# Performance work log

Hardware: AMD Instinct MI355X
Metric: run time of the kernel (lower is better)

Reference implementation:

```python
import jax, jax.numpy as jnp
import numpy as np

B, N, D_IN, D_OUT, E = 16, 16384, 128, 128, 65536
LN_EPS = 1e-5


def setup_inputs() -> dict:
    key = jax.random.key(0)
    k1, k2, k3, k4 = jax.random.split(key, 4)
    x = jax.random.normal(k1, (B, N, D_IN), dtype=jnp.float32)
    edge_index = jax.random.randint(k2, (2, E), 0, N, dtype=jnp.int64)
    W_self = jax.random.normal(k3, (D_OUT, D_IN), dtype=jnp.float32) / np.sqrt(D_IN)
    W_neigh = jax.random.normal(k4, (D_OUT, D_IN), dtype=jnp.float32) / np.sqrt(D_IN)
    return {
        "x": x,
        "edge_index": edge_index,
        "batch_size": B,
        "W_self": W_self,
        "W_neigh": W_neigh,
        "bias": jnp.zeros((D_OUT,), jnp.float32),
        "gamma": jnp.ones((D_OUT,), jnp.float32),
        "beta": jnp.zeros((D_OUT,), jnp.float32),
    }


def reference(x, edge_index, batch_size, W_self, W_neigh, bias, gamma, beta):
    b, n, d = x.shape
    src, dst = edge_index[0], edge_index[1]
    # expand edge index for disjoint batched graphs: add per-graph node offsets
    offsets = (jnp.arange(batch_size, dtype=src.dtype) * n)[:, None]  # [B,1]
    src_e = (src[None, :] + offsets).reshape(-1)  # [B*E]
    dst_e = (dst[None, :] + offsets).reshape(-1)
    x_flat = x.reshape(batch_size * n, d)
    # scatter-sum neighbor features and degrees, then mean
    agg = jax.ops.segment_sum(x_flat[src_e], dst_e, num_segments=batch_size * n)
    deg = jax.ops.segment_sum(jnp.ones_like(dst_e, dtype=x_flat.dtype), dst_e,
                              num_segments=batch_size * n)
    neigh = agg / jnp.maximum(deg, 1.0)[:, None]
    out = x_flat @ W_self.T + neigh @ W_neigh.T + bias  # [B*N, D_OUT]
    # LayerNorm over last dim
    mu = jnp.mean(out, axis=-1, keepdims=True)
    var = jnp.mean(jnp.square(out - mu), axis=-1, keepdims=True)
    out = (out - mu) * jax.lax.rsqrt(var + LN_EPS) * gamma + beta
    out = jax.nn.relu(out)
    return out.reshape(batch_size, n, -1)
```

## Files before the change

### kernel.cpp

```cpp
#include <hip/hip_runtime.h>
#include <hip/hip_bf16.h>
#include <stdint.h>

#define B_ 16
#define N_ 16384
#define D_ 128
#define E_ 65536

typedef __attribute__((ext_vector_type(8))) __bf16 bf16x8;
typedef __attribute__((ext_vector_type(4))) float f32x4;
typedef __attribute__((ext_vector_type(4))) _Float16 half4;

__device__ __forceinline__ uint16_t f2bf(float f) {
    union { float f; uint32_t u; } v;
    v.f = f;
    uint32_t u = v.u;
    uint32_t r = (u + 0x7fffu + ((u >> 16) & 1u)) >> 16;
    return (uint16_t)r;
}

__device__ __forceinline__ bool ei_is64(const int* __restrict__ ei, int t) {
    int w = ei[2 * (t & 63) + 1];
    return __ballot(w != 0) == 0ull;
}

__global__ void k_cntpack(const int* __restrict__ ei,
                          const float* __restrict__ wself,
                          const float* __restrict__ wneigh,
                          const float* __restrict__ x,
                          int* __restrict__ deg,
                          uint16_t* __restrict__ wpack,
                          _Float16* __restrict__ xh) {
    int t = threadIdx.x;
    int bid = blockIdx.x;
    if (bid < 256) {
        bool is64 = ei_is64(ei, t);
        int e = bid * 256 + t;
        int d = is64 ? ei[2 * (E_ + e)] : ei[E_ + e];
        atomicAdd(&deg[d], 1);
    } else if (bid < 384) {
        int g = (bid - 256) * 256 + t;
        int j = g & 7;
        int lane = (g >> 3) & 63;
        int nt = (g >> 9) & 7;
        int ks = g >> 12;
        int k = ks * 32 + (lane >> 4) * 8 + j;
        int n = nt * 16 + (lane & 15);
        float v = (k < 128) ? wself[n * 128 + k] : wneigh[n * 128 + (k - 128)];
        wpack[g] = f2bf(v);
    } else {
        size_t idx = (size_t)(bid - 384) * 2048 + (size_t)t * 8;
        const float4* p = (const float4*)(x + idx);
        float4 v0 = p[0], v1 = p[1];
        union { _Float16 hh[8]; uint4 u; } pk;
        pk.hh[0] = (_Float16)v0.x; pk.hh[1] = (_Float16)v0.y;
        pk.hh[2] = (_Float16)v0.z; pk.hh[3] = (_Float16)v0.w;
        pk.hh[4] = (_Float16)v1.x; pk.hh[5] = (_Float16)v1.y;
        pk.hh[6] = (_Float16)v1.z; pk.hh[7] = (_Float16)v1.w;
        *(uint4*)(xh + idx) = pk.u;
    }
}

__global__ void k_scan(const int* __restrict__ deg, int* __restrict__ off,
                       int* __restrict__ cur) {
    __shared__ int ps[256];
    int t = threadIdx.x;
    int vals[64];
    const int4* dv = (const int4*)(deg + t * 64);
    int s = 0;
#pragma unroll
    for (int i = 0; i < 16; i++) {
        int4 v = dv[i];
        vals[4 * i + 0] = v.x; vals[4 * i + 1] = v.y;
        vals[4 * i + 2] = v.z; vals[4 * i + 3] = v.w;
        s += v.x + v.y + v.z + v.w;
    }
    ps[t] = s;
    __syncthreads();
#pragma unroll
    for (int st = 1; st < 256; st <<= 1) {
        int add = (t >= st) ? ps[t - st] : 0;
        __syncthreads();
        ps[t] += add;
        __syncthreads();
    }
    int run = ps[t] - s;
#pragma unroll
    for (int i = 0; i < 64; i++) {
        off[t * 64 + i] = run;
        cur[t * 64 + i] = run;
        run += vals[i];
    }
    if (t == 255) off[N_] = run;
}

__global__ void k_fill(const int* __restrict__ ei, int* __restrict__ cur,
                       int* __restrict__ adj) {
    int t = threadIdx.x;
    bool is64 = ei_is64(ei, t);
    int e = blockIdx.x * 256 + t;
    int s = is64 ? ei[2 * e] : ei[e];
    int d = is64 ? ei[2 * (E_ + e)] : ei[E_ + e];
    int p = atomicAdd(&cur[d], 1);
    adj[p] = s;
}

template <bool USE_H>
__global__ __launch_bounds__(256, 8) void k_main(
    const float* __restrict__ x,
    const _Float16* __restrict__ xh,
    const int* __restrict__ off,
    const int* __restrict__ adj,
    const uint16_t* __restrict__ wpack,
    const float* __restrict__ bias,
    const float* __restrict__ gamma_,
    const float* __restrict__ beta_,
    float* __restrict__ out) {
    __shared__ __align__(16) unsigned char smem[16896];
    __shared__ float prm[3][128];
    uint16_t* As = (uint16_t*)smem;
    float* Cs = (float*)smem;

    int t = threadIdx.x;
    int b = blockIdx.x & 15;
    int tile = blockIdx.x >> 4;
    int node0 = tile * 32;

    if (t < 128) {
        prm[0][t] = bias[t];
        prm[1][t] = gamma_[t];
        prm[2][t] = beta_[t];
    }

    int r = t >> 3;
    int h = t & 7;
    int node = node0 + r;
    const size_t xrow = ((size_t)b * N_ + node) * D_;
    int mt = r >> 4, m = r & 15;

    int hw = t >> 5, l = t & 31;
    int obase = node0 + hw * 4;
    int oo[5];
#pragma unroll
    for (int i = 0; i < 5; i++) oo[i] = off[obase + i];

    if (USE_H) {
        const half4* xv = (const half4*)(xh + xrow);
#pragma unroll
        for (int c = 0; c < 2; c++) {
            half4 v0 = xv[h * 4 + 2 * c + 0];
            half4 v1 = xv[h * 4 + 2 * c + 1];
            float f[8] = {(float)v0.x, (float)v0.y, (float)v0.z, (float)v0.w,
                          (float)v1.x, (float)v1.y, (float)v1.z, (float)v1.w};
            uint32_t pk[4];
#pragma unroll
            for (int p = 0; p < 4; p++)
                pk[p] = (uint32_t)f2bf(f[2 * p]) | ((uint32_t)f2bf(f[2 * p + 1]) << 16);
            int kc = h * 2 + c, ks = kc >> 2, qd = kc & 3;
            *(uint4*)&As[(((ks * 2 + mt) * 64) + qd * 16 + m) * 8] =
                make_uint4(pk[0], pk[1], pk[2], pk[3]);
        }
    } else {
        const float4* xv = (const float4*)(x + xrow);
#pragma unroll
        for (int c = 0; c < 2; c++) {
            float4 a0 = xv[h * 4 + 2 * c + 0];
            float4 a1 = xv[h * 4 + 2 * c + 1];
            float f[8] = {a0.x, a0.y, a0.z, a0.w, a1.x, a1.y, a1.z, a1.w};
            uint32_t pk[4];
#pragma unroll
            for (int p = 0; p < 4; p++)
                pk[p] = (uint32_t)f2bf(f[2 * p]) | ((uint32_t)f2bf(f[2 * p + 1]) << 16);
            int kc = h * 2 + c, ks = kc >> 2, qd = kc & 3;
            *(uint4*)&As[(((ks * 2 + mt) * 64) + qd * 16 + m) * 8] =
                make_uint4(pk[0], pk[1], pk[2], pk[3]);
        }
    }

    {
#pragma unroll
        for (int i = 0; i < 4; i++) {
            int r2 = hw * 4 + i;
            int o0 = oo[i], o1 = oo[i + 1];
            float a0 = 0.f, a1 = 0.f, a2 = 0.f, a3 = 0.f;
            if (USE_H) {
                const _Float16* xg = xh + (size_t)b * N_ * D_;
                int e = o0;
                for (; e + 1 < o1; e += 2) {
                    int s0 = adj[e], s1 = adj[e + 1];
                    half4 v0 = *(const half4*)(xg + (size_t)s0 * D_ + l * 4);
                    half4 v1 = *(const half4*)(xg + (size_t)s1 * D_ + l * 4);
                    a0 += (float)v0.x + (float)v1.x;
                    a1 += (float)v0.y + (float)v1.y;
                    a2 += (float)v0.z + (float)v1.z;
                    a3 += (float)v0.w + (float)v1.w;
                }
                if (e < o1) {
                    int s0 = adj[e];
                    half4 v0 = *(const half4*)(xg + (size_t)s0 * D_ + l * 4);
                    a0 += (float)v0.x; a1 += (float)v0.y;
                    a2 += (float)v0.z; a3 += (float)v0.w;
                }
            } else {
                const float* xg = x + (size_t)b * N_ * D_;
                int e = o0;
                for (; e + 1 < o1; e += 2) {
                    int s0 = adj[e], s1 = adj[e + 1];
                    float4 v0 = *(const float4*)(xg + (size_t)s0 * D_ + l * 4);
                    float4 v1 = *(const float4*)(xg + (size_t)s1 * D_ + l * 4);
                    a0 += v0.x + v1.x; a1 += v0.y + v1.y;
                    a2 += v0.z + v1.z; a3 += v0.w + v1.w;
                }
                if (e < o1) {
                    int s0 = adj[e];
                    float4 v0 = *(const float4*)(xg + (size_t)s0 * D_ + l * 4);
                    a0 += v0.x; a1 += v0.y; a2 += v0.z; a3 += v0.w;
                }
            }
            float sc = 1.f / fmaxf((float)(o1 - o0), 1.f);
            int mt2 = r2 >> 4, m2 = r2 & 15;
            int kc = 16 + (l >> 1);
            int ks = kc >> 2, qd = kc & 3;
            uint2 pv;
            pv.x = (uint32_t)f2bf(a0 * sc) | ((uint32_t)f2bf(a1 * sc) << 16);
            pv.y = (uint32_t)f2bf(a2 * sc) | ((uint32_t)f2bf(a3 * sc) << 16);
            *(uint2*)&As[(((ks * 2 + mt2) * 64) + qd * 16 + m2) * 8 + (l & 1) * 4] = pv;
        }
    }

    __syncthreads();

    int wv = t >> 6;
    int lane = t & 63;
    f32x4 accv[2][2];
#pragma unroll
    for (int i = 0; i < 2; i++)
#pragma unroll
        for (int j = 0; j < 2; j++) {
            f32x4 z = {0.f, 0.f, 0.f, 0.f};
            accv[i][j] = z;
        }

    const uint4* wp = (const uint4*)wpack;
#pragma unroll
    for (int ks = 0; ks < 8; ks++) {
        uint4 b0u = wp[(ks * 8 + 2 * wv + 0) * 64 + lane];
        uint4 b1u = wp[(ks * 8 + 2 * wv + 1) * 64 + lane];
        bf16x8 bf0 = __builtin_bit_cast(bf16x8, b0u);
        bf16x8 bf1 = __builtin_bit_cast(bf16x8, b1u);
#pragma unroll
        for (int mtt = 0; mtt < 2; mtt++) {
            bf16x8 a = *(const bf16x8*)&As[((ks * 2 + mtt) * 64 + lane) * 8];
            accv[mtt][0] = __builtin_amdgcn_mfma_f32_16x16x32_bf16(a, bf0, accv[mtt][0], 0, 0, 0);
            accv[mtt][1] = __builtin_amdgcn_mfma_f32_16x16x32_bf16(a, bf1, accv[mtt][1], 0, 0, 0);
        }
    }

    __syncthreads();

#pragma unroll
    for (int mtt = 0; mtt < 2; mtt++)
#pragma unroll
        for (int ntl = 0; ntl < 2; ntl++)
#pragma unroll
            for (int rg = 0; rg < 4; rg++) {
                int row = mtt * 16 + (lane >> 4) * 4 + rg;
                int col = (2 * wv + ntl) * 16 + (lane & 15);
                Cs[row * 132 + (col >> 5) * 33 + (col & 31)] = accv[mtt][ntl][rg];
            }

    __syncthreads();

    {
        int cbase = r * 132 + (h >> 1) * 33 + (h & 1) * 16;
        float s1 = 0.f, s2 = 0.f;
#pragma unroll
        for (int i = 0; i < 16; i++) {
            float v = Cs[cbase + i] + prm[0][h * 16 + i];
            s1 += v;
            s2 += v * v;
        }
        s1 += __shfl_xor(s1, 1, 64);
        s2 += __shfl_xor(s2, 1, 64);
        s1 += __shfl_xor(s1, 2, 64);
        s2 += __shfl_xor(s2, 2, 64);
        s1 += __shfl_xor(s1, 4, 64);
        s2 += __shfl_xor(s2, 4, 64);
        float mu = s1 * (1.f / 128.f);
        float var = s2 * (1.f / 128.f) - mu * mu;
        float rstd = rsqrtf(var + 1e-5f);

        float* orow = out + xrow;
#pragma unroll
        for (int c = 0; c < 4; c++) {
            float4 o;
            float tmp[4];
#pragma unroll
            for (int j = 0; j < 4; j++) {
                int i0 = c * 4 + j;
                int d0 = h * 16 + i0;
                float v = Cs[cbase + i0] + prm[0][d0];
                tmp[j] = fmaxf((v - mu) * rstd * prm[1][d0] + prm[2][d0], 0.f);
            }
            o.x = tmp[0]; o.y = tmp[1]; o.z = tmp[2]; o.w = tmp[3];
            *(float4*)&orow[h * 16 + c * 4] = o;
        }
    }
}

extern "C" void kernel_launch(void* const* d_in, const int* in_sizes, int n_in,
                              void* d_out, int out_size, void* d_ws, size_t ws_size,
                              hipStream_t stream) {
    (void)in_sizes; (void)n_in; (void)out_size;
    const float* x      = (const float*)d_in[0];
    const int*   ei     = (const int*)d_in[1];
    const float* wself  = (const float*)d_in[3];
    const float* wneigh = (const float*)d_in[4];
    const float* bias   = (const float*)d_in[5];
    const float* gma    = (const float*)d_in[6];
    const float* bta    = (const float*)d_in[7];
    float* out = (float*)d_out;

    char* ws = (char*)d_ws;
    int* deg        = (int*)(ws);
    int* off        = (int*)(ws + 65536);
    int* cur        = (int*)(ws + 131584);
    int* adj        = (int*)(ws + 197120);
    uint16_t* wpack = (uint16_t*)(ws + 459264);
    _Float16* xh    = (_Float16*)(ws + 524800);

    bool use_h = d_ws != nullptr &&
                 ws_size >= (size_t)524800 + (size_t)B_ * N_ * D_ * 2;

    hipMemsetAsync(deg, 0, N_ * sizeof(int), stream);
    k_cntpack<<<use_h ? 16768 : 384, 256, 0, stream>>>(ei, wself, wneigh, x, deg,
                                                       wpack, xh);
    k_scan<<<1, 256, 0, stream>>>(deg, off, cur);
    k_fill<<<E_ / 256, 256, 0, stream>>>(ei, cur, adj);
    if (use_h)
        k_main<true><<<B_ * (N_ / 32), 256, 0, stream>>>(x, xh, off, adj, wpack,
                                                         bias, gma, bta, out);
    else
        k_main<false><<<B_ * (N_ / 32), 256, 0, stream>>>(x, xh, off, adj, wpack,
                                                          bias, gma, bta, out);
}
```

Measured before the change: 351.0 us.

## Widen gather loads, swizzle LDS tile, remap blocks to XCDs, coarsen fp16 convert

The neighbor gather now reads 16-byte half8 rows per lane, with two half-waves splitting the edges and combining through a shuffle, instead of 8-byte loads. The A tile in LDS uses an XOR-swizzled layout to avoid bank conflicts on the wider stores. Block IDs are remapped so each XCD handles a fixed set of batch graphs, which is meant to improve L2 locality of the gathered rows. The fp32-to-fp16 conversion kernel also processes four chunks per thread, so it launches fewer blocks. The costs are an extra shuffle reduction per node and idle lanes during the final write.

```diff
diff --git a/kernel.cpp b/kernel.cpp
--- a/kernel.cpp
+++ b/kernel.cpp
@@ -10,6 +10,7 @@
 typedef __attribute__((ext_vector_type(8))) __bf16 bf16x8;
 typedef __attribute__((ext_vector_type(4))) float f32x4;
 typedef __attribute__((ext_vector_type(4))) _Float16 half4;
+typedef __attribute__((ext_vector_type(8))) _Float16 half8;
 
 __device__ __forceinline__ uint16_t f2bf(float f) {
     union { float f; uint32_t u; } v;
@@ -17,6 +18,11 @@
     uint32_t u = v.u;
     uint32_t r = (u + 0x7fffu + ((u >> 16) & 1u)) >> 16;
     return (uint16_t)r;
+}
+
+__device__ __forceinline__ int As_off(int ch, int l16) {
+    int c = (ch & 7) ^ ((l16 >> 4) & 1);
+    return ch * 1024 + ((l16 ^ c) << 4);
 }
 
 __device__ __forceinline__ bool ei_is64(const int* __restrict__ ei, int t) {
@@ -49,15 +55,19 @@
         float v = (k < 128) ? wself[n * 128 + k] : wneigh[n * 128 + (k - 128)];
         wpack[g] = f2bf(v);
     } else {
-        size_t idx = (size_t)(bid - 384) * 2048 + (size_t)t * 8;
-        const float4* p = (const float4*)(x + idx);
-        float4 v0 = p[0], v1 = p[1];
-        union { _Float16 hh[8]; uint4 u; } pk;
-        pk.hh[0] = (_Float16)v0.x; pk.hh[1] = (_Float16)v0.y;
-        pk.hh[2] = (_Float16)v0.z; pk.hh[3] = (_Float16)v0.w;
-        pk.hh[4] = (_Float16)v1.x; pk.hh[5] = (_Float16)v1.y;
-        pk.hh[6] = (_Float16)v1.z; pk.hh[7] = (_Float16)v1.w;
-        *(uint4*)(xh + idx) = pk.u;
+        size_t base = (size_t)(bid - 384) * 8192 + (size_t)t * 8;
+#pragma unroll
+        for (int it = 0; it < 4; it++) {
+            size_t idx = base + (size_t)it * 2048;
+            const float4* p = (const float4*)(x + idx);
+            float4 v0 = p[0], v1 = p[1];
+            union { _Float16 hh[8]; uint4 u; } pk;
+            pk.hh[0] = (_Float16)v0.x; pk.hh[1] = (_Float16)v0.y;
+            pk.hh[2] = (_Float16)v0.z; pk.hh[3] = (_Float16)v0.w;
+            pk.hh[4] = (_Float16)v1.x; pk.hh[5] = (_Float16)v1.y;
+            pk.hh[6] = (_Float16)v1.z; pk.hh[7] = (_Float16)v1.w;
+            *(uint4*)(xh + idx) = pk.u;
+        }
     }
 }
 
@@ -118,12 +128,15 @@
     float* __restrict__ out) {
     __shared__ __align__(16) unsigned char smem[16896];
     __shared__ float prm[3][128];
-    uint16_t* As = (uint16_t*)smem;
+    unsigned char* Asb = smem;
     float* Cs = (float*)smem;
 
     int t = threadIdx.x;
-    int b = blockIdx.x & 15;
-    int tile = blockIdx.x >> 4;
+    int bid = blockIdx.x;
+    int xcd = bid & 7;
+    int w = bid >> 12;
+    int tile = (bid >> 3) & 511;
+    int b = w * 8 + xcd;
     int node0 = tile * 32;
 
     if (t < 128) {
@@ -132,99 +145,80 @@
         prm[2][t] = beta_[t];
     }
 
-    int r = t >> 3;
-    int h = t & 7;
-    int node = node0 + r;
-    const size_t xrow = ((size_t)b * N_ + node) * D_;
-    int mt = r >> 4, m = r & 15;
-
     int hw = t >> 5, l = t & 31;
+    int p = l >> 4;
+    int dl = l & 15;
+
     int obase = node0 + hw * 4;
     int oo[5];
 #pragma unroll
     for (int i = 0; i < 5; i++) oo[i] = off[obase + i];
 
-    if (USE_H) {
-        const half4* xv = (const half4*)(xh + xrow);
-#pragma unroll
-        for (int c = 0; c < 2; c++) {
-            half4 v0 = xv[h * 4 + 2 * c + 0];
-            half4 v1 = xv[h * 4 + 2 * c + 1];
-            float f[8] = {(float)v0.x, (float)v0.y, (float)v0.z, (float)v0.w,
-                          (float)v1.x, (float)v1.y, (float)v1.z, (float)v1.w};
+    const _Float16* xgb = xh + (size_t)b * N_ * D_;
+    const float* xgf = x + (size_t)b * N_ * D_;
+
+#pragma unroll
+    for (int i = 0; i < 2; i++) {
+        int r2 = hw * 4 + i * 2 + p;
+        int nd = node0 + r2;
+        float f[8];
+        if (USE_H) {
+            uint4 raw = *(const uint4*)(xgb + (size_t)nd * D_ + dl * 8);
+            half8 hv = __builtin_bit_cast(half8, raw);
+#pragma unroll
+            for (int j = 0; j < 8; j++) f[j] = (float)hv[j];
+        } else {
+            const float4* pv = (const float4*)(xgf + (size_t)nd * D_ + dl * 8);
+            float4 a0 = pv[0], a1 = pv[1];
+            f[0] = a0.x; f[1] = a0.y; f[2] = a0.z; f[3] = a0.w;
+            f[4] = a1.x; f[5] = a1.y; f[6] = a1.z; f[7] = a1.w;
+        }
+        uint32_t pk[4];
+#pragma unroll
+        for (int j = 0; j < 4; j++)
+            pk[j] = (uint32_t)f2bf(f[2 * j]) | ((uint32_t)f2bf(f[2 * j + 1]) << 16);
+        int ks = dl >> 2, qd = dl & 3;
+        int mt2 = r2 >> 4, m2 = r2 & 15;
+        *(uint4*)(Asb + As_off(ks * 2 + mt2, qd * 16 + m2)) =
+            make_uint4(pk[0], pk[1], pk[2], pk[3]);
+    }
+
+#pragma unroll
+    for (int i = 0; i < 4; i++) {
+        int r2 = hw * 4 + i;
+        int o0 = oo[i], o1 = oo[i + 1];
+        float a[8] = {0.f, 0.f, 0.f, 0.f, 0.f, 0.f, 0.f, 0.f};
+        if (USE_H) {
+            for (int e = o0 + p; e < o1; e += 2) {
+                int s0 = adj[e];
+                uint4 raw = *(const uint4*)(xgb + (size_t)s0 * D_ + dl * 8);
+                half8 hv = __builtin_bit_cast(half8, raw);
+#pragma unroll
+                for (int j = 0; j < 8; j++) a[j] += (float)hv[j];
+            }
+        } else {
+            for (int e = o0 + p; e < o1; e += 2) {
+                int s0 = adj[e];
+                const float4* pv = (const float4*)(xgf + (size_t)s0 * D_ + dl * 8);
+                float4 v0 = pv[0], v1 = pv[1];
+                a[0] += v0.x; a[1] += v0.y; a[2] += v0.z; a[3] += v0.w;
+                a[4] += v1.x; a[5] += v1.y; a[6] += v1.z; a[7] += v1.w;
+            }
+        }
+#pragma unroll
+        for (int j = 0; j < 8; j++) a[j] += __shfl_xor(a[j], 16, 64);
+        if (p == 0) {
+            float sc = 1.f / fmaxf((float)(o1 - o0), 1.f);
             uint32_t pk[4];
 #pragma unroll
-            for (int p = 0; p < 4; p++)
-                pk[p] = (uint32_t)f2bf(f[2 * p]) | ((uint32_t)f2bf(f[2 * p + 1]) << 16);
-            int kc = h * 2 + c, ks = kc >> 2, qd = kc & 3;
-            *(uint4*)&As[(((ks * 2 + mt) * 64) + qd * 16 + m) * 8] =
+            for (int j = 0; j < 4; j++)
+                pk[j] = (uint32_t)f2bf(a[2 * j] * sc) |
+                        ((uint32_t)f2bf(a[2 * j + 1] * sc) << 16);
+            int kc = 16 + dl;
+            int ks = kc >> 2, qd = kc & 3;
+            int mt2 = r2 >> 4, m2 = r2 & 15;
+            *(uint4*)(Asb + As_off(ks * 2 + mt2, qd * 16 + m2)) =
                 make_uint4(pk[0], pk[1], pk[2], pk[3]);
-        }
-    } else {
-        const float4* xv = (const float4*)(x + xrow);
-#pragma unroll
-        for (int c = 0; c < 2; c++) {
-            float4 a0 = xv[h * 4 + 2 * c + 0];
-            float4 a1 = xv[h * 4 + 2 * c + 1];
-            float f[8] = {a0.x, a0.y, a0.z, a0.w, a1.x, a1.y, a1.z, a1.w};
-            uint32_t pk[4];
-#pragma unroll
-            for (int p = 0; p < 4; p++)
-                pk[p] = (uint32_t)f2bf(f[2 * p]) | ((uint32_t)f2bf(f[2 * p + 1]) << 16);
-            int kc = h * 2 + c, ks = kc >> 2, qd = kc & 3;
-            *(uint4*)&As[(((ks * 2 + mt) * 64) + qd * 16 + m) * 8] =
-                make_uint4(pk[0], pk[1], pk[2], pk[3]);
-        }
-    }
-
-    {
-#pragma unroll
-        for (int i = 0; i < 4; i++) {
-            int r2 = hw * 4 + i;
-            int o0 = oo[i], o1 = oo[i + 1];
-            float a0 = 0.f, a1 = 0.f, a2 = 0.f, a3 = 0.f;
-            if (USE_H) {
-                const _Float16* xg = xh + (size_t)b * N_ * D_;
-                int e = o0;
-                for (; e + 1 < o1; e += 2) {
-                    int s0 = adj[e], s1 = adj[e + 1];
-                    half4 v0 = *(const half4*)(xg + (size_t)s0 * D_ + l * 4);
-                    half4 v1 = *(const half4*)(xg + (size_t)s1 * D_ + l * 4);
-                    a0 += (float)v0.x + (float)v1.x;
-                    a1 += (float)v0.y + (float)v1.y;
-                    a2 += (float)v0.z + (float)v1.z;
-                    a3 += (float)v0.w + (float)v1.w;
-                }
-                if (e < o1) {
-                    int s0 = adj[e];
-                    half4 v0 = *(const half4*)(xg + (size_t)s0 * D_ + l * 4);
-                    a0 += (float)v0.x; a1 += (float)v0.y;
-                    a2 += (float)v0.z; a3 += (float)v0.w;
-                }
-            } else {
-                const float* xg = x + (size_t)b * N_ * D_;
-                int e = o0;
-                for (; e + 1 < o1; e += 2) {
-                    int s0 = adj[e], s1 = adj[e + 1];
-                    float4 v0 = *(const float4*)(xg + (size_t)s0 * D_ + l * 4);
-                    float4 v1 = *(const float4*)(xg + (size_t)s1 * D_ + l * 4);
-                    a0 += v0.x + v1.x; a1 += v0.y + v1.y;
-                    a2 += v0.z + v1.z; a3 += v0.w + v1.w;
-                }
-                if (e < o1) {
-                    int s0 = adj[e];
-                    float4 v0 = *(const float4*)(xg + (size_t)s0 * D_ + l * 4);
-                    a0 += v0.x; a1 += v0.y; a2 += v0.z; a3 += v0.w;
-                }
-            }
-            float sc = 1.f / fmaxf((float)(o1 - o0), 1.f);
-            int mt2 = r2 >> 4, m2 = r2 & 15;
-            int kc = 16 + (l >> 1);
-            int ks = kc >> 2, qd = kc & 3;
-            uint2 pv;
-            pv.x = (uint32_t)f2bf(a0 * sc) | ((uint32_t)f2bf(a1 * sc) << 16);
-            pv.y = (uint32_t)f2bf(a2 * sc) | ((uint32_t)f2bf(a3 * sc) << 16);
-            *(uint2*)&As[(((ks * 2 + mt2) * 64) + qd * 16 + m2) * 8 + (l & 1) * 4] = pv;
         }
     }
 
@@ -250,7 +244,7 @@
         bf16x8 bf1 = __builtin_bit_cast(bf16x8, b1u);
 #pragma unroll
         for (int mtt = 0; mtt < 2; mtt++) {
-            bf16x8 a = *(const bf16x8*)&As[((ks * 2 + mtt) * 64 + lane) * 8];
+            bf16x8 a = *(const bf16x8*)(Asb + As_off(ks * 2 + mtt, lane));
             accv[mtt][0] = __builtin_amdgcn_mfma_f32_16x16x32_bf16(a, bf0, accv[mtt][0], 0, 0, 0);
             accv[mtt][1] = __builtin_amdgcn_mfma_f32_16x16x32_bf16(a, bf1, accv[mtt][1], 0, 0, 0);
         }
@@ -272,6 +266,10 @@
     __syncthreads();
 
     {
+        int r = t >> 3;
+        int h = t & 7;
+        int node = node0 + r;
+        const size_t xrow = ((size_t)b * N_ + node) * D_;
         int cbase = r * 132 + (h >> 1) * 33 + (h & 1) * 16;
         float s1 = 0.f, s2 = 0.f;
 #pragma unroll
@@ -333,8 +331,8 @@
                  ws_size >= (size_t)524800 + (size_t)B_ * N_ * D_ * 2;
 
     hipMemsetAsync(deg, 0, N_ * sizeof(int), stream);
-    k_cntpack<<<use_h ? 16768 : 384, 256, 0, stream>>>(ei, wself, wneigh, x, deg,
-                                                       wpack, xh);
+    k_cntpack<<<use_h ? 4480 : 384, 256, 0, stream>>>(ei, wself, wneigh, x, deg,
+                                                      wpack, xh);
     k_scan<<<1, 256, 0, stream>>>(deg, off, cur);
     k_fill<<<E_ / 256, 256, 0, stream>>>(ei, cur, adj);
     if (use_h)
```

Measured after the change: 336.5 us. 1.04x faster.
